# Performance work log

Hardware: AMD Instinct MI355X
Metric: run time of the kernel (lower is better)

## Reference

```python
import jax, jax.numpy as jnp
import numpy as np
import math

BLUR_K = [1.0, 3.0, 3.0, 1.0]
EPS = 1e-8


def _make_blur_kernel(upsample_factor=2):
    k = jnp.asarray(BLUR_K, dtype=jnp.float32)
    k = k[None, :] * k[:, None]
    k = k / k.sum()
    return k * (upsample_factor ** 2)


def setup_inputs() -> dict:
    key = jax.random.key(0)
    ks = jax.random.split(key, 5)
    B, Cin, Cout, K, S, H, W = 16, 256, 128, 3, 512, 64, 64
    x = jax.random.normal(ks[0], (B, Cin, H, W), dtype=jnp.float32)
    style = jax.random.normal(ks[1], (B, S), dtype=jnp.float32)
    weight = jax.random.normal(ks[2], (1, Cout, Cin, K, K), dtype=jnp.float32)
    mod_w = jax.random.normal(ks[3], (Cin, S), dtype=jnp.float32) * (1.0 / math.sqrt(S))
    mod_b = jnp.ones((Cin,), dtype=jnp.float32)  # StyleGAN2 modulation bias init = 1
    return {"x": x, "style": style, "weight": weight, "mod_w": mod_w, "mod_b": mod_b}


def reference(x, style, weight, mod_w, mod_b):
    B, Cin, H, W = x.shape
    Cout = weight.shape[1]
    K = weight.shape[-1]
    scale = 1.0 / math.sqrt(Cin * K * K)

    # modulation: Linear(style_dim -> in_channel)
    s = style @ mod_w.T + mod_b                      # (B, Cin)
    w = scale * weight * s[:, None, :, None, None]   # (B, Cout, Cin, K, K)
    demod = jax.lax.rsqrt(jnp.sum(w * w, axis=(2, 3, 4)) + EPS)  # (B, Cout)
    w = w * demod[:, :, None, None, None]

    # per-sample conv_transpose2d(stride=2, padding=0, groups=B)
    # == lhs-dilated grouped correlation with spatially-flipped kernel
    kernel = jnp.flip(w, axis=(3, 4)).reshape(B * Cout, Cin, K, K)
    xg = x.reshape(1, B * Cin, H, W)
    out = jax.lax.conv_general_dilated(
        xg, kernel,
        window_strides=(1, 1),
        padding=((K - 1, K - 1), (K - 1, K - 1)),
        lhs_dilation=(2, 2),
        feature_group_count=B,
        dimension_numbers=("NCHW", "OIHW", "NCHW"),
    )  # (1, B*Cout, 2H+K-2, 2W+K-2) -> here (1, B*Cout, 2H+1, 2W+1)
    Ht, Wt = out.shape[2], out.shape[3]

    # Blur2 / upfirdn2d(up=1, down=1, pad=(pad0, pad1))
    # p = len(blur_kernel) - 2 - (K - 1); pad0 = (p+1)//2 + 1; pad1 = p//2 + 1
    p = len(BLUR_K) - 2 - (K - 1)
    pad0 = (p + 1) // 2 + 1
    pad1 = p // 2 + 1
    bk = _make_blur_kernel()                       # (4, 4)
    bw = jnp.flip(bk, axis=(0, 1))[None, None]     # (1, 1, 4, 4)
    outs = out.reshape(B * Cout, 1, Ht, Wt)
    blurred = jax.lax.conv_general_dilated(
        outs, bw,
        window_strides=(1, 1),
        padding=((pad0, pad1), (pad0, pad1)),
        dimension_numbers=("NCHW", "OIHW", "NCHW"),
    )
    Hb, Wb = blurred.shape[2], blurred.shape[3]
    return blurred.reshape(B, Cout, Hb, Wb)
```

## Files before the change

kernel.cpp:

```cpp
#include <hip/hip_runtime.h>
#include <stdint.h>

#define CIN 256
#define COUT 128
#define SDIM 512
#define NB 16

#define XP_RSTRIDE 16896
#define XP_BSTRIDE 1115136
#define A_BSTRIDE (512*2304)

typedef __attribute__((ext_vector_type(8))) short short8;
typedef __attribute__((ext_vector_type(4))) float f32x4;

__device__ __forceinline__ float bf2f(unsigned short h) {
  union { unsigned int u; float f; } v; v.u = ((unsigned int)h) << 16; return v.f;
}
__device__ __forceinline__ unsigned short f2bf(float f) {
  union { float f; unsigned int u; } v; v.f = f;
  return (unsigned short)((v.u + 0x7fffu + ((v.u >> 16) & 1u)) >> 16);
}
__device__ __forceinline__ void gll16(const void* g, void* l) {
  __builtin_amdgcn_global_load_lds(
      (const __attribute__((address_space(1))) unsigned int*)g,
      (__attribute__((address_space(3))) unsigned int*)l, 16, 0, 0);
}

__global__ __launch_bounds__(256) void k_detect(
    const unsigned short* __restrict__ xr, int* __restrict__ flag) {
  __shared__ int red[4];
  int t = threadIdx.x, cnt = 0;
  for (int i = t; i < 8192; i += 256) {
    int e = (xr[2*i] >> 7) & 0xff;
    cnt += (e > 90 && e < 145) ? 1 : 0;
  }
  #pragma unroll
  for (int off = 32; off > 0; off >>= 1) cnt += __shfl_down(cnt, off);
  if ((t & 63) == 0) red[t >> 6] = cnt;
  __syncthreads();
  if (t == 0) *flag = (red[0] + red[1] + red[2] + red[3] < 5000) ? 1 : 0;
}

__global__ __launch_bounds__(256) void k_style(
    const void* __restrict__ style_v, const void* __restrict__ mod_w_v,
    const void* __restrict__ mod_b_v, const int* __restrict__ flag,
    float* __restrict__ s_out) {
  __shared__ float st[SDIM];
  int b = blockIdx.x, t = threadIdx.x;
  int isf = *flag;
  float acc;
  if (!isf) {
    const unsigned short* style = (const unsigned short*)style_v;
    const unsigned short* mod_w = (const unsigned short*)mod_w_v;
    const unsigned short* mod_b = (const unsigned short*)mod_b_v;
    st[t]       = bf2f(style[b*SDIM + t]);
    st[t + 256] = bf2f(style[b*SDIM + t + 256]);
    __syncthreads();
    const uint4* wr = (const uint4*)(mod_w + (size_t)t*SDIM);
    acc = bf2f(mod_b[t]);
    #pragma unroll 4
    for (int s8 = 0; s8 < SDIM/8; ++s8) {
      uint4 p = wr[s8];
      int sb = s8*8;
      acc += bf2f((unsigned short)(p.x & 0xffff))*st[sb]
           + bf2f((unsigned short)(p.x >> 16))   *st[sb+1]
           + bf2f((unsigned short)(p.y & 0xffff))*st[sb+2]
           + bf2f((unsigned short)(p.y >> 16))   *st[sb+3]
           + bf2f((unsigned short)(p.z & 0xffff))*st[sb+4]
           + bf2f((unsigned short)(p.z >> 16))   *st[sb+5]
           + bf2f((unsigned short)(p.w & 0xffff))*st[sb+6]
           + bf2f((unsigned short)(p.w >> 16))   *st[sb+7];
    }
  } else {
    const float* style = (const float*)style_v;
    const float* mod_w = (const float*)mod_w_v;
    const float* mod_b = (const float*)mod_b_v;
    st[t]       = style[b*SDIM + t];
    st[t + 256] = style[b*SDIM + t + 256];
    __syncthreads();
    const float4* wr = (const float4*)(mod_w + (size_t)t*SDIM);
    acc = mod_b[t];
    #pragma unroll 4
    for (int s4 = 0; s4 < SDIM/4; ++s4) {
      float4 p = wr[s4];
      int sb = s4*4;
      acc += p.x*st[sb] + p.y*st[sb+1] + p.z*st[sb+2] + p.w*st[sb+3];
    }
  }
  s_out[b*CIN + t] = acc;
}

__global__ __launch_bounds__(256) void k_weights(
    const void* __restrict__ weight_v,
    const float* __restrict__ s_in,
    const int* __restrict__ flag,
    unsigned short* __restrict__ Aw) {
  int co = blockIdx.x, b = blockIdx.y, ci = threadIdx.x;
  int isf = *flag;
  float sm = 0.0208333333333333f * s_in[b*CIN + ci];
  float w9[9]; float ss = 0.f;
  if (!isf) {
    const unsigned short* wp = (const unsigned short*)weight_v + ((size_t)co*CIN + ci)*9;
    #pragma unroll
    for (int k = 0; k < 9; ++k) { float v = bf2f(wp[k]) * sm; w9[k] = v; ss += v*v; }
  } else {
    const float* wp = (const float*)weight_v + ((size_t)co*CIN + ci)*9;
    #pragma unroll
    for (int k = 0; k < 9; ++k) { float v = wp[k] * sm; w9[k] = v; ss += v*v; }
  }
  #pragma unroll
  for (int off = 32; off > 0; off >>= 1) ss += __shfl_down(ss, off);
  __shared__ float red[4];
  if ((ci & 63) == 0) red[ci >> 6] = ss;
  __syncthreads();
  float demod = rsqrtf(red[0] + red[1] + red[2] + red[3] + 1e-8f);
  #pragma unroll
  for (int k = 0; k < 9; ++k) w9[k] *= demod;
  const float F[4] = {0.25f, 0.75f, 0.75f, 0.25f};
  float C6[6][6];
  #pragma unroll
  for (int ty = 0; ty < 6; ++ty) {
    #pragma unroll
    for (int tx = 0; tx < 6; ++tx) {
      float acc = 0.f;
      #pragma unroll
      for (int ay = 0; ay < 3; ++ay) {
        int fy = ay - ty + 3;
        if (fy < 0 || fy > 3) continue;
        float ra = 0.f;
        #pragma unroll
        for (int ax = 0; ax < 3; ++ax) {
          int fx = ax - tx + 3;
          if (fx < 0 || fx > 3) continue;
          ra += w9[ay*3 + ax] * F[fx];
        }
        acc += ra * F[fy];
      }
      C6[ty][tx] = acc;
    }
  }
  unsigned short* Ab = Aw + (size_t)b*A_BSTRIDE;
  #pragma unroll
  for (int py = 0; py < 2; ++py) {
    #pragma unroll
    for (int px = 0; px < 2; ++px) {
      unsigned short* Am = Ab + (size_t)(py*256 + co*2 + px)*2304 + ci;
      #pragma unroll
      for (int dh = -1; dh <= 1; ++dh) {
        #pragma unroll
        for (int dw = -1; dw <= 1; ++dw) {
          int tap = (dh+1)*3 + (dw+1);
          Am[tap*256] = f2bf(C6[py - 2*dh + 2][px - 2*dw + 2]);
        }
      }
    }
  }
}

__global__ __launch_bounds__(256) void k_transpose(
    const void* __restrict__ x_v,
    const int* __restrict__ flag,
    unsigned short* __restrict__ xp) {
  int r_out = blockIdx.x, b = blockIdx.y, t = threadIdx.x;
  unsigned short* rp = xp + (size_t)b*XP_BSTRIDE + (size_t)r_out*XP_RSTRIDE;
  int r_in = r_out - 1;
  if (r_in < 0 || r_in >= 64) {
    uint4 z = make_uint4(0,0,0,0);
    #pragma unroll
    for (int i = 0; i < 9; ++i) {
      int idx = i*256 + t;
      if (idx < 2112) ((uint4*)rp)[idx] = z;
    }
    return;
  }
  if (t < 64) {
    uint4 z = make_uint4(0,0,0,0);
    int col = (t < 32) ? 0 : 65;
    ((uint4*)(rp + col*256))[t & 31] = z;
  }
  int isf = *flag;
  __shared__ unsigned int lds32[64*33];
  int tci = t >> 3;
  int tc8 = t & 7;
  int cS  = t >> 2;
  int jg  = t & 3;
  for (int g4 = 0; g4 < 4; ++g4) {
    int ci0 = g4 * 64;
    int ci = ci0 + tci*2;
    size_t base = (((size_t)b*CIN + ci)*64 + r_in)*64 + tc8*8;
    unsigned int v[8];
    if (isf) {
      const float* s0 = (const float*)x_v + base;
      const float* s1 = s0 + 4096;
      float4 a0 = ((const float4*)s0)[0], a1 = ((const float4*)s0)[1];
      float4 b0 = ((const float4*)s1)[0], b1 = ((const float4*)s1)[1];
      v[0] = f2bf(a0.x) | ((unsigned int)f2bf(b0.x) << 16);
      v[1] = f2bf(a0.y) | ((unsigned int)f2bf(b0.y) << 16);
      v[2] = f2bf(a0.z) | ((unsigned int)f2bf(b0.z) << 16);
      v[3] = f2bf(a0.w) | ((unsigned int)f2bf(b0.w) << 16);
      v[4] = f2bf(a1.x) | ((unsigned int)f2bf(b1.x) << 16);
      v[5] = f2bf(a1.y) | ((unsigned int)f2bf(b1.y) << 16);
      v[6] = f2bf(a1.z) | ((unsigned int)f2bf(b1.z) << 16);
      v[7] = f2bf(a1.w) | ((unsigned int)f2bf(b1.w) << 16);
    } else {
      const unsigned short* s0 = (const unsigned short*)x_v + base;
      const unsigned short* s1 = s0 + 4096;
      union { uint4 q; unsigned short h[8]; } u0, u1;
      u0.q = *(const uint4*)s0; u1.q = *(const uint4*)s1;
      #pragma unroll
      for (int j = 0; j < 8; ++j)
        v[j] = (unsigned int)u0.h[j] | ((unsigned int)u1.h[j] << 16);
    }
    if (g4) __syncthreads();
    #pragma unroll
    for (int j = 0; j < 8; ++j)
      lds32[(tc8*8 + j)*33 + tci] = v[j];
    __syncthreads();
    union { unsigned int o[8]; uint4 q[2]; } ob;
    #pragma unroll
    for (int w = 0; w < 8; ++w)
      ob.o[w] = lds32[cS*33 + jg*8 + w];
    uint4* dst = (uint4*)(rp + (size_t)(cS+1)*256 + ci0 + jg*16);
    dst[0] = ob.q[0];
    dst[1] = ob.q[1];
  }
}

__global__ __launch_bounds__(256) void k_gemm(
    const unsigned short* __restrict__ Aw,
    const unsigned short* __restrict__ xp,
    const int* __restrict__ flag,
    void* __restrict__ out) {
  __shared__ __align__(16) unsigned short As[2][128*32];
  __shared__ __align__(16) unsigned short Bs[2][128*32];
  int g = blockIdx.x;
  int b  = ((g & 7) << 1) | ((g >> 3) & 1);
  int mt = (g >> 4) & 3;
  int nt = g >> 6;
  int yy0 = nt << 1;
  int t = threadIdx.x;
  int wave = t >> 6, lane = t & 63;
  int row = t >> 2, part = t & 3;
  int isf = *flag;

  int partS = part ^ ((row >> 2) & 3);
  int dstOff = row*32 + part*8;
  const unsigned short* pA0 = Aw + (size_t)b*A_BSTRIDE + (size_t)(mt*128 + row)*2304 + partS*8;
  const unsigned short* pA1 = pA0 + (size_t)64*2304;
  const unsigned short* pB0 = xp + (size_t)b*XP_BSTRIDE + (size_t)(yy0 + 1)*XP_RSTRIDE
                              + (size_t)(row + 1)*256 + partS*8;

  f32x4 acc[4][4];
  #pragma unroll
  for (int i = 0; i < 4; ++i)
    #pragma unroll
    for (int j = 0; j < 4; ++j)
      acc[i][j] = (f32x4){0.f, 0.f, 0.f, 0.f};

  int mb = (wave >> 1) << 6;
  int nb = (wave & 1) << 6;
  int l15 = lane & 15, q = lane >> 4;
  int qs = q ^ ((l15 >> 2) & 3);

  #define STAGE(BI, A0, A1, B0, KK) { \
    gll16((A0) + (KK)*32, &As[BI][dstOff]); \
    gll16((A1) + (KK)*32, &As[BI][dstOff + 2048]); \
    gll16((B0) + (KK)*32, &Bs[BI][dstOff]); \
    gll16((B0) + (KK)*32 + XP_RSTRIDE, &Bs[BI][dstOff + 2048]); \
  }

  #define COMPUTE(BI) { \
    short8 af[4], bv[4]; \
    _Pragma("unroll") \
    for (int i_ = 0; i_ < 4; ++i_) \
      af[i_] = *(const short8*)&As[BI][(mb + i_*16 + l15)*32 + qs*8]; \
    _Pragma("unroll") \
    for (int j_ = 0; j_ < 4; ++j_) \
      bv[j_] = *(const short8*)&Bs[BI][(nb + j_*16 + l15)*32 + qs*8]; \
    _Pragma("unroll") \
    for (int i_ = 0; i_ < 4; ++i_) \
      _Pragma("unroll") \
      for (int j_ = 0; j_ < 4; ++j_) \
        acc[i_][j_] = __builtin_amdgcn_mfma_f32_16x16x32_bf16(af[i_], bv[j_], acc[i_][j_], 0, 0, 0); \
  }

  STAGE(0, pA0, pA1, pB0 - XP_RSTRIDE - 256, 0);
  __syncthreads();

  for (int tap = 0; tap < 9; ++tap) {
    int dh  = (tap >= 6) ? 1 : ((tap >= 3) ? 0 : -1);
    int dwx = tap - (dh + 1)*3 - 1;
    const unsigned short* a0 = pA0 + tap*256;
    const unsigned short* a1 = pA1 + tap*256;
    const unsigned short* b0 = pB0 + dh*XP_RSTRIDE + dwx*256;
    int tap1 = tap + 1;
    int dh1  = (tap1 >= 6) ? 1 : ((tap1 >= 3) ? 0 : -1);
    int dwx1 = tap1 - (dh1 + 1)*3 - 1;
    const unsigned short* nb0 = pB0 + dh1*XP_RSTRIDE + dwx1*256;
    #pragma unroll
    for (int kk = 0; kk < 8; kk += 2) {
      STAGE(1, a0, a1, b0, kk + 1);
      COMPUTE(0);
      __syncthreads();
      if (kk < 6) {
        STAGE(0, a0, a1, b0, kk + 2);
      } else if (tap < 8) {
        STAGE(0, a0 + 256, a1 + 256, nb0, 0);
      }
      COMPUTE(1);
      if (!(tap == 8 && kk == 6)) __syncthreads();
    }
  }
  #undef STAGE
  #undef COMPUTE

  int py = mt >> 1;
  int ry = wave & 1;
  int y = ((yy0 + ry) << 1) + py;
  int cobase = ((mt & 1) << 6) + ((wave >> 1) << 5);
  #pragma unroll
  for (int i = 0; i < 4; ++i) {
    #pragma unroll
    for (int rr = 0; rr < 2; ++rr) {
      int co = cobase + i*8 + q*2 + rr;
      size_t obase = (((size_t)b*COUT + co)*128 + y)*64;
      if (!isf) {
        unsigned int* outp = (unsigned int*)out;
        #pragma unroll
        for (int j = 0; j < 4; ++j) {
          unsigned int pk = (unsigned int)f2bf(acc[i][j][rr*2])
                          | ((unsigned int)f2bf(acc[i][j][rr*2 + 1]) << 16);
          outp[obase + j*16 + l15] = pk;
        }
      } else {
        float2* outp = (float2*)out;
        #pragma unroll
        for (int j = 0; j < 4; ++j)
          outp[obase + j*16 + l15] = make_float2(acc[i][j][rr*2], acc[i][j][rr*2 + 1]);
      }
    }
  }
}

extern "C" void kernel_launch(void* const* d_in, const int* in_sizes, int n_in,
                              void* d_out, int out_size, void* d_ws, size_t ws_size,
                              hipStream_t stream) {
  const void* x      = d_in[0];
  const void* style  = d_in[1];
  const void* weight = d_in[2];
  const void* mod_w  = d_in[3];
  const void* mod_b  = d_in[4];
  char* ws = (char*)d_ws;
  int* flag           = (int*)ws;
  float* s_buf        = (float*)(ws + 1024);
  unsigned short* Aw  = (unsigned short*)(ws + 32768);
  unsigned short* xpd = (unsigned short*)(ws + 32768 + 37748736);

  k_detect   <<<1, 256, 0, stream>>>((const unsigned short*)x, flag);
  k_style    <<<NB, 256, 0, stream>>>(style, mod_w, mod_b, flag, s_buf);
  k_weights  <<<dim3(COUT, NB), 256, 0, stream>>>(weight, s_buf, flag, Aw);
  k_transpose<<<dim3(66, NB), 256, 0, stream>>>(x, flag, xpd);
  k_gemm     <<<2048, 256, 0, stream>>>(Aw, xpd, flag, d_out);
}
```

Baseline: 431.1 us.

## Enlarge GEMM tile to 256x256 with 8 waves and explicit phased pipeline

The implicit-GEMM kernel moves from 128x128 tiles with 4 waves to 256x256 tiles with 8 waves, halving K-step granularity to 64 and using a 4-phase schedule per K tile. Each phase interleaves LDS reads, async global-to-LDS loads for future stages and MFMA bursts, controlled by explicit vmcnt/lgkmcnt waits, sched barriers and setprio. The aim is more data reuse per loaded byte and better overlap of memory with matrix math. The cost is higher register pressure (128 accumulators per thread), 64KB of LDS, and fewer blocks (512), which may hurt occupancy or load balance.

```diff
diff --git a/kernel.cpp b/kernel.cpp
--- a/kernel.cpp
+++ b/kernel.cpp
@@ -226,120 +226,166 @@
   }
 }
 
-__global__ __launch_bounds__(256) void k_gemm(
+__global__ __launch_bounds__(512, 2) void k_gemm(
     const unsigned short* __restrict__ Aw,
     const unsigned short* __restrict__ xp,
     const int* __restrict__ flag,
     void* __restrict__ out) {
-  __shared__ __align__(16) unsigned short As[2][128*32];
-  __shared__ __align__(16) unsigned short Bs[2][128*32];
+  __shared__ __align__(16) unsigned short As[2][2][8192];
+  __shared__ __align__(16) unsigned short Bs[2][2][8192];
   int g = blockIdx.x;
   int b  = ((g & 7) << 1) | ((g >> 3) & 1);
-  int mt = (g >> 4) & 3;
-  int nt = g >> 6;
-  int yy0 = nt << 1;
+  int mt = (g >> 4) & 1;
+  int nt = g >> 5;
+  int yy0 = nt << 2;
   int t = threadIdx.x;
   int wave = t >> 6, lane = t & 63;
+  int wm = wave >> 2, wn = wave & 3;
+  int wh = wn >> 1, wr = wn & 1;
+  int l15 = lane & 15, q = lane >> 4;
+  int qs = q ^ ((l15 >> 2) & 3);
+  int lOff = l15*32 + qs*8;
   int row = t >> 2, part = t & 3;
+  int partS = part ^ ((row >> 2) & 3);
+  int dst8 = t * 8;
   int isf = *flag;
 
-  int partS = part ^ ((row >> 2) & 3);
-  int dstOff = row*32 + part*8;
-  const unsigned short* pA0 = Aw + (size_t)b*A_BSTRIDE + (size_t)(mt*128 + row)*2304 + partS*8;
-  const unsigned short* pA1 = pA0 + (size_t)64*2304;
-  const unsigned short* pB0 = xp + (size_t)b*XP_BSTRIDE + (size_t)(yy0 + 1)*XP_RSTRIDE
-                              + (size_t)(row + 1)*256 + partS*8;
-
-  f32x4 acc[4][4];
-  #pragma unroll
-  for (int i = 0; i < 4; ++i)
+  const unsigned short* pA0 = Aw + (size_t)b*A_BSTRIDE + (size_t)(mt*256 + row)*2304 + partS*8;
+  const unsigned short* pA1 = pA0 + (size_t)128*2304;
+  const unsigned short* pB0 = xp + (size_t)b*XP_BSTRIDE
+      + (size_t)(yy0 + (row >> 6) + 1)*XP_RSTRIDE + (size_t)((row & 63) + 1)*256 + partS*8;
+  const unsigned short* pB1 = pB0 + (size_t)2*XP_RSTRIDE;
+
+  f32x4 acc[8][4];
+  #pragma unroll
+  for (int i = 0; i < 8; ++i)
     #pragma unroll
     for (int j = 0; j < 4; ++j)
       acc[i][j] = (f32x4){0.f, 0.f, 0.f, 0.f};
 
-  int mb = (wave >> 1) << 6;
-  int nb = (wave & 1) << 6;
-  int l15 = lane & 15, q = lane >> 4;
-  int qs = q ^ ((l15 >> 2) & 3);
-
-  #define STAGE(BI, A0, A1, B0, KK) { \
-    gll16((A0) + (KK)*32, &As[BI][dstOff]); \
-    gll16((A1) + (KK)*32, &As[BI][dstOff + 2048]); \
-    gll16((B0) + (KK)*32, &Bs[BI][dstOff]); \
-    gll16((B0) + (KK)*32 + XP_RSTRIDE, &Bs[BI][dstOff + 2048]); \
-  }
-
-  #define COMPUTE(BI) { \
-    short8 af[4], bv[4]; \
+  #define BARR() do { asm volatile("" ::: "memory"); __builtin_amdgcn_s_barrier(); \
+                      __builtin_amdgcn_sched_barrier(0); } while (0)
+  #define LGKM0() do { asm volatile("s_waitcnt lgkmcnt(0)" ::: "memory"); \
+                       __builtin_amdgcn_sched_barrier(0); } while (0)
+  #define WVM8() do { asm volatile("s_waitcnt vmcnt(8)" ::: "memory"); \
+                      __builtin_amdgcn_sched_barrier(0); } while (0)
+  #define WVM4() do { asm volatile("s_waitcnt vmcnt(4)" ::: "memory"); \
+                      __builtin_amdgcn_sched_barrier(0); } while (0)
+  #define WVM0() do { asm volatile("s_waitcnt vmcnt(0)" ::: "memory"); \
+                      __builtin_amdgcn_sched_barrier(0); } while (0)
+
+  #define STG_A(D, H, KH, KT) gll16(pA##H + (KT)*64 + (KH)*32, &As[D][H][(KH)*4096 + dst8]);
+  #define STG_B(D, H, KH, KT, DH, DW) \
+    gll16(pB##H + (DH)*XP_RSTRIDE + (DW)*256 + ((KT)&3)*64 + (KH)*32, \
+          &Bs[D][H][(KH)*4096 + dst8]);
+
+  #define PH_READ_B(D, KH) { \
+    _Pragma("unroll") \
+    for (int j_ = 0; j_ < 4; ++j_) \
+      bv[j_] = *(const short8*)&Bs[D][wh][(KH)*4096 + wr*2048 + j_*512 + lOff]; }
+  #define PH_READ_A(D, KH, MQ) { \
     _Pragma("unroll") \
     for (int i_ = 0; i_ < 4; ++i_) \
-      af[i_] = *(const short8*)&As[BI][(mb + i_*16 + l15)*32 + qs*8]; \
+      af[i_] = *(const short8*)&As[D][wm][(KH)*4096 + (MQ)*2048 + i_*512 + lOff]; }
+  #define PH_MFMA(MQ) { \
+    __builtin_amdgcn_s_setprio(1); \
     _Pragma("unroll") \
     for (int j_ = 0; j_ < 4; ++j_) \
-      bv[j_] = *(const short8*)&Bs[BI][(nb + j_*16 + l15)*32 + qs*8]; \
-    _Pragma("unroll") \
-    for (int i_ = 0; i_ < 4; ++i_) \
       _Pragma("unroll") \
-      for (int j_ = 0; j_ < 4; ++j_) \
-        acc[i_][j_] = __builtin_amdgcn_mfma_f32_16x16x32_bf16(af[i_], bv[j_], acc[i_][j_], 0, 0, 0); \
-  }
-
-  STAGE(0, pA0, pA1, pB0 - XP_RSTRIDE - 256, 0);
-  __syncthreads();
-
-  for (int tap = 0; tap < 9; ++tap) {
-    int dh  = (tap >= 6) ? 1 : ((tap >= 3) ? 0 : -1);
-    int dwx = tap - (dh + 1)*3 - 1;
-    const unsigned short* a0 = pA0 + tap*256;
-    const unsigned short* a1 = pA1 + tap*256;
-    const unsigned short* b0 = pB0 + dh*XP_RSTRIDE + dwx*256;
-    int tap1 = tap + 1;
-    int dh1  = (tap1 >= 6) ? 1 : ((tap1 >= 3) ? 0 : -1);
-    int dwx1 = tap1 - (dh1 + 1)*3 - 1;
-    const unsigned short* nb0 = pB0 + dh1*XP_RSTRIDE + dwx1*256;
-    #pragma unroll
-    for (int kk = 0; kk < 8; kk += 2) {
-      STAGE(1, a0, a1, b0, kk + 1);
-      COMPUTE(0);
-      __syncthreads();
-      if (kk < 6) {
-        STAGE(0, a0, a1, b0, kk + 2);
-      } else if (tap < 8) {
-        STAGE(0, a0 + 256, a1 + 256, nb0, 0);
-      }
-      COMPUTE(1);
-      if (!(tap == 8 && kk == 6)) __syncthreads();
-    }
-  }
-  #undef STAGE
-  #undef COMPUTE
-
-  int py = mt >> 1;
-  int ry = wave & 1;
-  int y = ((yy0 + ry) << 1) + py;
-  int cobase = ((mt & 1) << 6) + ((wave >> 1) << 5);
-  #pragma unroll
-  for (int i = 0; i < 4; ++i) {
-    #pragma unroll
-    for (int rr = 0; rr < 2; ++rr) {
-      int co = cobase + i*8 + q*2 + rr;
-      size_t obase = (((size_t)b*COUT + co)*128 + y)*64;
-      if (!isf) {
-        unsigned int* outp = (unsigned int*)out;
+      for (int i_ = 0; i_ < 4; ++i_) \
+        acc[(MQ)*4 + i_][j_] = __builtin_amdgcn_mfma_f32_16x16x32_bf16( \
+            af[i_], bv[j_], acc[(MQ)*4 + i_][j_], 0, 0, 0); \
+    __builtin_amdgcn_s_setprio(0); \
+    __builtin_amdgcn_sched_barrier(0); }
+
+  #define TILE(KT, D, E, DO1, DO0, WMID, WEND, DOEND) { \
+    const int kt1_ = (KT) + 1, kt2_ = (KT) + 2; \
+    int tap1_ = kt1_ >> 2; \
+    int dh1_ = (tap1_ >= 6) ? 1 : ((tap1_ >= 3) ? 0 : -1); \
+    int dw1_ = tap1_ - (dh1_ + 1)*3 - 1; \
+    int tap2_ = kt2_ >> 2; \
+    int dh2_ = (tap2_ >= 6) ? 1 : ((tap2_ >= 3) ? 0 : -1); \
+    int dw2_ = tap2_ - (dh2_ + 1)*3 - 1; \
+    short8 af[4], bv[4]; \
+     \
+    PH_READ_B(D, 0); PH_READ_A(D, 0, 0); \
+    if (DO1) { STG_A(E, 0, 1, kt1_); STG_A(E, 1, 1, kt1_); } \
+    BARR(); LGKM0(); PH_MFMA(0); BARR(); \
+     \
+    PH_READ_A(D, 0, 1); \
+    if (DO1) { STG_B(E, 0, 1, kt1_, dh1_, dw1_); STG_B(E, 1, 1, kt1_, dh1_, dw1_); } \
+    BARR(); LGKM0(); PH_MFMA(1); \
+    WMID; BARR(); \
+     \
+    PH_READ_B(D, 1); PH_READ_A(D, 1, 0); \
+    if (DO0) { STG_A(D, 0, 0, kt2_); STG_A(D, 1, 0, kt2_); } \
+    BARR(); LGKM0(); PH_MFMA(0); BARR(); \
+     \
+    PH_READ_A(D, 1, 1); \
+    if (DO0) { STG_B(D, 0, 0, kt2_, dh2_, dw2_); STG_B(D, 1, 0, kt2_, dh2_, dw2_); } \
+    BARR(); LGKM0(); PH_MFMA(1); \
+    if (DOEND) { WEND; BARR(); } \
+  }
+
+  STG_A(0, 0, 0, 0); STG_A(0, 1, 0, 0);
+  STG_B(0, 0, 0, 0, -1, -1); STG_B(0, 1, 0, 0, -1, -1);
+  STG_A(0, 0, 1, 0); STG_A(0, 1, 1, 0);
+  STG_B(0, 0, 1, 0, -1, -1); STG_B(0, 1, 1, 0, -1, -1);
+  STG_A(1, 0, 0, 1); STG_A(1, 1, 0, 1);
+  STG_B(1, 0, 0, 1, -1, -1); STG_B(1, 1, 0, 1, -1, -1);
+  WVM8(); BARR();
+
+  #pragma unroll 1
+  for (int kt = 0; kt < 34; kt += 2) {
+    TILE(kt,     0, 1, 1, 1, WVM8(), WVM8(), 1);
+    TILE(kt + 1, 1, 0, 1, 1, WVM8(), WVM8(), 1);
+  }
+  TILE(34, 0, 1, 1, 0, WVM8(), WVM4(), 1);
+  TILE(35, 1, 0, 0, 0, WVM0(), WVM0(), 0);
+
+  #undef TILE
+  #undef PH_MFMA
+  #undef PH_READ_A
+  #undef PH_READ_B
+  #undef STG_B
+  #undef STG_A
+
+  int y = 8*nt + 2*wn + mt;
+  if (!isf) {
+    unsigned int* outp = (unsigned int*)out;
+    #pragma unroll
+    for (int ig = 0; ig < 8; ++ig) {
+      #pragma unroll
+      for (int rr = 0; rr < 2; ++rr) {
+        int co = wm*64 + (ig >> 2)*32 + (ig & 3)*8 + q*2 + rr;
+        size_t obase = (((size_t)b*COUT + co)*128 + y)*64;
         #pragma unroll
         for (int j = 0; j < 4; ++j) {
-          unsigned int pk = (unsigned int)f2bf(acc[i][j][rr*2])
-                          | ((unsigned int)f2bf(acc[i][j][rr*2 + 1]) << 16);
+          unsigned int pk = (unsigned int)f2bf(acc[ig][j][rr*2])
+                          | ((unsigned int)f2bf(acc[ig][j][rr*2 + 1]) << 16);
           outp[obase + j*16 + l15] = pk;
         }
-      } else {
-        float2* outp = (float2*)out;
+      }
+    }
+  } else {
+    float2* outp = (float2*)out;
+    #pragma unroll
+    for (int ig = 0; ig < 8; ++ig) {
+      #pragma unroll
+      for (int rr = 0; rr < 2; ++rr) {
+        int co = wm*64 + (ig >> 2)*32 + (ig & 3)*8 + q*2 + rr;
+        size_t obase = (((size_t)b*COUT + co)*128 + y)*64;
         #pragma unroll
         for (int j = 0; j < 4; ++j)
-          outp[obase + j*16 + l15] = make_float2(acc[i][j][rr*2], acc[i][j][rr*2 + 1]);
+          outp[obase + j*16 + l15] = make_float2(acc[ig][j][rr*2], acc[ig][j][rr*2 + 1]);
       }
     }
   }
+  #undef BARR
+  #undef LGKM0
+  #undef WVM8
+  #undef WVM4
+  #undef WVM0
 }
 
 extern "C" void kernel_launch(void* const* d_in, const int* in_sizes, int n_in,
@@ -360,5 +406,5 @@
   k_style    <<<NB, 256, 0, stream>>>(style, mod_w, mod_b, flag, s_buf);
   k_weights  <<<dim3(COUT, NB), 256, 0, stream>>>(weight, s_buf, flag, Aw);
   k_transpose<<<dim3(66, NB), 256, 0, stream>>>(x, flag, xpd);
-  k_gemm     <<<2048, 256, 0, stream>>>(Aw, xpd, flag, d_out);
-}
+  k_gemm     <<<512, 512, 0, stream>>>(Aw, xpd, flag, d_out);
+}
```

Result: faster. 386.5 us (-10.4%).
